# Kernel optimization log

Hardware: AMD Instinct MI355X
Metric: run time of the kernel (lower is better)

## Reference

```python
import jax, jax.numpy as jnp
import numpy as np

N = 16384
HID = 256
MI = 128
POS_PER_NODE = 4
TEMP = 0.5


def setup_inputs() -> dict:
    key = jax.random.key(0)
    k1, k2, k3, k4 = jax.random.split(key, 4)
    h_v1 = jax.random.normal(k1, (N, HID), dtype=jnp.float32)
    h_v2 = jax.random.normal(k2, (N, HID), dtype=jnp.float32)
    W = jax.random.normal(k3, (HID, MI), dtype=jnp.float32) * (1.0 / np.sqrt(HID))
    b = jnp.zeros((MI,), dtype=jnp.float32)
    # 4 positives per row -> every row has a nonzero positive count
    pos_row = jnp.repeat(jnp.arange(N, dtype=jnp.int32), POS_PER_NODE)
    pos_col = jax.random.randint(k4, (N * POS_PER_NODE,), 0, N, dtype=jnp.int32)
    return {"h_v1": h_v1, "h_v2": h_v2, "W": W, "b": b,
            "pos_row": pos_row, "pos_col": pos_col}


def _l2norm(x):
    return x / jnp.linalg.norm(x, axis=-1, keepdims=True)


def _cal_loss_mi(e1, e2, pos_row, pos_col):
    # sim_mat[i,j] = <e1_i, e2_j> / T   (N x N, the big intermediate)
    sim = jnp.einsum('ik,jk->ij', e1, e2) / TEMP
    sim = sim - jax.lax.stop_gradient(jnp.max(sim, axis=1, keepdims=True))
    sim = jnp.exp(sim)
    sim_pos = sim[pos_row, pos_col]                      # [E] gather
    row_sum = jnp.sum(sim, axis=1)                       # [N]
    pos_sum = jax.ops.segment_sum(sim_pos, pos_row, num_segments=N)
    denom = (row_sum - pos_sum)[pos_row]                 # [E]
    log_lv = jnp.log(sim_pos / denom)                    # [E]
    pos_cnt = jax.ops.segment_sum(jnp.ones_like(sim_pos), pos_row, num_segments=N)
    per_row = jax.ops.segment_sum(log_lv, pos_row, num_segments=N) / pos_cnt
    return -jnp.mean(per_row)


def reference(h_v1, h_v2, W, b, pos_row, pos_col):
    p1 = _l2norm(jax.nn.relu(h_v1 @ W + b))
    p2 = _l2norm(jax.nn.relu(h_v2 @ W + b))
    loss = 0.5 * (_cal_loss_mi(p1, p2, pos_row, pos_col)
                  + _cal_loss_mi(p2, p1, pos_row, pos_col))
    return loss
```

## Files before the change

### kernel.cpp

```cpp
#include <hip/hip_runtime.h>

typedef unsigned short ushort_t;
typedef unsigned int uint32;
typedef __attribute__((ext_vector_type(8))) short short8;
typedef __attribute__((ext_vector_type(4))) float f32x4;
typedef __attribute__((ext_vector_type(2))) float f32x2;

#define HID 256
#define MI 128
#define ALPHA 2.8853900817779268f
#define LN2F 0.69314718055994531f

__device__ __forceinline__ float bflo(uint32 u) { return __uint_as_float(u << 16); }
__device__ __forceinline__ float bfhi(uint32 u) { return __uint_as_float(u & 0xffff0000u); }
__device__ __forceinline__ ushort_t f2bf(float f) {
  uint32 u = __float_as_uint(f);
  u += 0x7fffu + ((u >> 16) & 1u);
  return (ushort_t)(u >> 16);
}

__global__ __launch_bounds__(256) void prep_kernel(
    const float* __restrict__ W, ushort_t* __restrict__ Wtb,
    float* __restrict__ fbase, int nz, float* __restrict__ out)
{
  int idx = blockIdx.x * 256 + threadIdx.x;
  if (idx < HID * MI) {
    int k = idx >> 7, nn = idx & 127;
    Wtb[nn * HID + k] = f2bf(W[k * MI + nn]);
  }
  if (idx < nz) fbase[idx] = 0.f;
  if (idx == 0) out[0] = 0.f;
}

__global__ __launch_bounds__(256) void proj_kernel(
    const float* __restrict__ h1, const float* __restrict__ h2,
    const ushort_t* __restrict__ Wtb, const float* __restrict__ b,
    ushort_t* __restrict__ p1b, ushort_t* __restrict__ p2b, int n)
{
  __shared__ __align__(16) unsigned char hb[64 * 512];
  int t = threadIdx.x;
  int lane = t & 63, w = t >> 6;
  int lr = lane & 15, lg = lane >> 4;
  long R0 = (long)blockIdx.x * 64;
  const float* src = (R0 < n) ? (h1 + R0 * HID) : (h2 + (R0 - n) * HID);
  ushort_t* dst = (R0 < n) ? (p1b + R0 * MI) : (p2b + (R0 - n) * MI);
  float scale = (R0 < n) ? ALPHA : 1.0f;

  float bb[8];
  #pragma unroll
  for (int ch = 0; ch < 8; ++ch) bb[ch] = b[ch * 16 + lr];

  const float4* g4 = (const float4*)src;
  #pragma unroll
  for (int i = 0; i < 16; ++i) {
    int idx4 = i * 256 + t;
    float4 v = g4[idx4];
    int row = idx4 >> 6;
    int k0 = (idx4 & 63) * 4;
    int gr = k0 >> 3;
    int off = row * 512 + ((gr ^ (row & 15)) << 4) + (k0 & 7) * 2;
    uint32 lo = (uint32)f2bf(v.x) | ((uint32)f2bf(v.y) << 16);
    uint32 hi = (uint32)f2bf(v.z) | ((uint32)f2bf(v.w) << 16);
    uint2 pk; pk.x = lo; pk.y = hi;
    *(uint2*)(hb + off) = pk;
  }
  __syncthreads();

  short8 afr[8];
  #pragma unroll
  for (int kt = 0; kt < 8; ++kt) {
    int row = w * 16 + lr;
    int g = kt * 4 + lg;
    afr[kt] = *(const short8*)(hb + row * 512 + ((g ^ (row & 15)) << 4));
  }

  f32x4 acc[8];
  #pragma unroll
  for (int ch = 0; ch < 8; ++ch) acc[ch] = (f32x4){0.f, 0.f, 0.f, 0.f};
  #pragma unroll
  for (int ch = 0; ch < 8; ++ch) {
    #pragma unroll
    for (int kt = 0; kt < 8; ++kt) {
      short8 bf = *(const short8*)(Wtb + (size_t)(ch * 16 + lr) * HID + kt * 32 + lg * 8);
      acc[ch] = __builtin_amdgcn_mfma_f32_16x16x32_bf16(afr[kt], bf, acc[ch], 0, 0, 0);
    }
  }

  #pragma unroll
  for (int r = 0; r < 4; ++r) {
    float v[8];
    float ss = 0.f;
    #pragma unroll
    for (int ch = 0; ch < 8; ++ch) {
      v[ch] = fmaxf(acc[ch][r] + bb[ch], 0.f);
      ss += v[ch] * v[ch];
    }
    ss += __shfl_xor(ss, 1, 64);
    ss += __shfl_xor(ss, 2, 64);
    ss += __shfl_xor(ss, 4, 64);
    ss += __shfl_xor(ss, 8, 64);
    float rn = rsqrtf(ss) * scale;
    int row = w * 16 + lg * 4 + r;
    #pragma unroll
    for (int ch = 0; ch < 8; ++ch)
      dst[(size_t)row * MI + ch * 16 + lr] = f2bf(v[ch] * rn);
  }
}

__global__ __launch_bounds__(512, 4) void sim_kernel(
    const ushort_t* __restrict__ p1b, const ushort_t* __restrict__ p2b,
    float* __restrict__ rowsum, float* __restrict__ colsum)
{
  __shared__ __align__(16) unsigned char ldsB[32768];
  __shared__ float colacc[1024];
  int t = threadIdx.x;
  int lane = t & 63, w = t >> 6;
  int lr = lane & 15, lg = lane >> 4;
  int rowbase = blockIdx.y * 256 + w * 32;
  int jbase = blockIdx.x * 1024;

  uint4 st0, st1;
  int g0 = t, g1 = t + 512;
  int row0 = g0 >> 4, gs0 = g0 & 15;
  int row1 = g1 >> 4, gs1 = g1 & 15;

  auto load_stage = [&](int jt) {
    int j0 = jbase + jt * 64;
    st0 = *(const uint4*)(p2b + (size_t)(j0 + row0) * MI + (gs0 << 3));
    st1 = *(const uint4*)(p2b + (size_t)(j0 + row1) * MI + (gs1 << 3));
  };
  auto write_stage = [&](int buf) {
    *(uint4*)(ldsB + buf * 16384 + row0 * 256 + ((gs0 ^ (row0 & 15)) << 4)) = st0;
    *(uint4*)(ldsB + buf * 16384 + row1 * 256 + ((gs1 ^ (row1 & 15)) << 4)) = st1;
  };

  load_stage(0);

  short8 afr[2][4];
  #pragma unroll
  for (int rt = 0; rt < 2; ++rt)
    #pragma unroll
    for (int kt = 0; kt < 4; ++kt)
      afr[rt][kt] = *(const short8*)(p1b + (size_t)(rowbase + rt * 16 + lr) * MI + kt * 32 + lg * 8);

  colacc[t] = 0.f;
  colacc[512 + t] = 0.f;

  f32x2 rs2[2][2];
  #pragma unroll
  for (int rt = 0; rt < 2; ++rt) {
    rs2[rt][0] = (f32x2){0.f, 0.f};
    rs2[rt][1] = (f32x2){0.f, 0.f};
  }

  write_stage(0);
  __syncthreads();

  for (int jt = 0; jt < 16; ++jt) {
    int cur = jt & 1;
    if (jt + 1 < 16) load_stage(jt + 1);
    const unsigned char* B = ldsB + cur * 16384;

    #pragma unroll
    for (int ch = 0; ch < 4; ++ch) {
      f32x4 acc[2];
      acc[0] = (f32x4){0.f, 0.f, 0.f, 0.f};
      acc[1] = (f32x4){0.f, 0.f, 0.f, 0.f};
      #pragma unroll
      for (int kt = 0; kt < 4; ++kt) {
        int ncol = ch * 16 + lr;
        int g = kt * 4 + lg;
        short8 bf = *(const short8*)(B + ncol * 256 + ((g ^ (ncol & 15)) << 4));
        acc[0] = __builtin_amdgcn_mfma_f32_16x16x32_bf16(afr[0][kt], bf, acc[0], 0, 0, 0);
        acc[1] = __builtin_amdgcn_mfma_f32_16x16x32_bf16(afr[1][kt], bf, acc[1], 0, 0, 0);
      }
      f32x2 cs2 = (f32x2){0.f, 0.f};
      #pragma unroll
      for (int rt = 0; rt < 2; ++rt) {
        f32x2 e01, e23;
        e01[0] = __builtin_amdgcn_exp2f(acc[rt][0]);
        e01[1] = __builtin_amdgcn_exp2f(acc[rt][1]);
        e23[0] = __builtin_amdgcn_exp2f(acc[rt][2]);
        e23[1] = __builtin_amdgcn_exp2f(acc[rt][3]);
        rs2[rt][0] += e01;
        rs2[rt][1] += e23;
        cs2 += e01;
        cs2 += e23;
      }
      float csum = cs2[0] + cs2[1];
      csum += __shfl_xor(csum, 16, 64);
      csum += __shfl_xor(csum, 32, 64);
      if (lg == 0) atomicAdd(&colacc[jt * 64 + ch * 16 + lr], csum);
    }
    if (jt + 1 < 16) write_stage(1 - cur);
    __syncthreads();
  }

  #pragma unroll
  for (int rt = 0; rt < 2; ++rt)
    #pragma unroll
    for (int j = 0; j < 2; ++j)
      #pragma unroll
      for (int s = 0; s < 2; ++s) {
        float v = rs2[rt][j][s];
        v += __shfl_xor(v, 1, 64);
        v += __shfl_xor(v, 2, 64);
        v += __shfl_xor(v, 4, 64);
        v += __shfl_xor(v, 8, 64);
        if (lr == 0) atomicAdd(&rowsum[rowbase + rt * 16 + lg * 4 + j * 2 + s], v);
      }

  atomicAdd(&colsum[jbase + t], colacc[t]);
  atomicAdd(&colsum[jbase + 512 + t], colacc[512 + t]);
}

__global__ __launch_bounds__(256) void edge_kernel(
    const int* __restrict__ pos_row, const int* __restrict__ pos_col,
    const ushort_t* __restrict__ p1b, const ushort_t* __restrict__ p2b,
    float* __restrict__ psum1, float* __restrict__ psum2,
    float* __restrict__ srow1, float* __restrict__ srow2,
    float* __restrict__ cntb, int E)
{
  int tid = blockIdx.x * 256 + threadIdx.x;
  int e = tid >> 2, q = tid & 3;
  if (e >= E) return;
  int r = pos_row[e], c = pos_col[e];
  const uint4* a1 = (const uint4*)(p1b + (size_t)r * MI) + q * 4;
  const uint4* b1 = (const uint4*)(p2b + (size_t)c * MI) + q * 4;
  const uint4* a2 = (const uint4*)(p1b + (size_t)c * MI) + q * 4;
  const uint4* b2 = (const uint4*)(p2b + (size_t)r * MI) + q * 4;
  float d1 = 0.f, d2 = 0.f;
  #pragma unroll
  for (int it = 0; it < 4; ++it) {
    uint4 x = a1[it], y = b1[it];
    d1 += bflo(x.x) * bflo(y.x) + bfhi(x.x) * bfhi(y.x);
    d1 += bflo(x.y) * bflo(y.y) + bfhi(x.y) * bfhi(y.y);
    d1 += bflo(x.z) * bflo(y.z) + bfhi(x.z) * bfhi(y.z);
    d1 += bflo(x.w) * bflo(y.w) + bfhi(x.w) * bfhi(y.w);
    uint4 u = a2[it], v = b2[it];
    d2 += bflo(u.x) * bflo(v.x) + bfhi(u.x) * bfhi(v.x);
    d2 += bflo(u.y) * bflo(v.y) + bfhi(u.y) * bfhi(v.y);
    d2 += bflo(u.z) * bflo(v.z) + bfhi(u.z) * bfhi(v.z);
    d2 += bflo(u.w) * bflo(v.w) + bfhi(u.w) * bfhi(v.w);
  }
  d1 += __shfl_xor(d1, 1, 64);
  d1 += __shfl_xor(d1, 2, 64);
  d2 += __shfl_xor(d2, 1, 64);
  d2 += __shfl_xor(d2, 2, 64);
  if (q == 0) {
    float e1 = __builtin_amdgcn_exp2f(d1);
    float e2 = __builtin_amdgcn_exp2f(d2);
    atomicAdd(&psum1[r], e1);
    atomicAdd(&srow1[r], d1 * LN2F);
    atomicAdd(&psum2[r], e2);
    atomicAdd(&srow2[r], d2 * LN2F);
    atomicAdd(&cntb[r], 1.0f);
  }
}

__global__ __launch_bounds__(256) void finalize_kernel(
    const float* __restrict__ rowsum, const float* __restrict__ colsum,
    const float* __restrict__ psum1, const float* __restrict__ psum2,
    const float* __restrict__ srow1, const float* __restrict__ srow2,
    const float* __restrict__ cntb, float* __restrict__ out, int n)
{
  __shared__ float sred[4];
  int r = blockIdx.x * 256 + threadIdx.x;
  float local = 0.f;
  if (r < n) {
    float inv = 1.0f / cntb[r];
    float d1 = rowsum[r] - psum1[r];
    float d2 = colsum[r] - psum2[r];
    local = srow1[r] * inv - __builtin_amdgcn_logf(d1) * LN2F
          + srow2[r] * inv - __builtin_amdgcn_logf(d2) * LN2F;
  }
  #pragma unroll
  for (int m = 1; m <= 32; m <<= 1) local += __shfl_xor(local, m, 64);
  int lane = threadIdx.x & 63, wv = threadIdx.x >> 6;
  if (lane == 0) sred[wv] = local;
  __syncthreads();
  if (threadIdx.x == 0) {
    float tot = sred[0] + sred[1] + sred[2] + sred[3];
    atomicAdd(out, -tot / (2.0f * n));
  }
}

extern "C" void kernel_launch(void* const* d_in, const int* in_sizes, int n_in,
                              void* d_out, int out_size, void* d_ws, size_t ws_size,
                              hipStream_t stream)
{
  const float* h1 = (const float*)d_in[0];
  const float* h2 = (const float*)d_in[1];
  const float* W  = (const float*)d_in[2];
  const float* b  = (const float*)d_in[3];
  const int* pos_row = (const int*)d_in[4];
  const int* pos_col = (const int*)d_in[5];
  int n = in_sizes[0] / HID;
  int E = in_sizes[4];
  float* out = (float*)d_out;

  char* ws = (char*)d_ws;
  ushort_t* p1b = (ushort_t*)ws;
  ushort_t* p2b = p1b + (size_t)n * MI;
  float* fbase  = (float*)(ws + (size_t)2 * n * MI * sizeof(ushort_t));
  float* rowsum = fbase;
  float* colsum = rowsum + n;
  float* psum1  = colsum + n;
  float* psum2  = psum1 + n;
  float* srow1  = psum2 + n;
  float* srow2  = srow1 + n;
  float* cntb   = srow2 + n;
  ushort_t* Wtb = (ushort_t*)(cntb + n);

  int nz = 7 * n;
  prep_kernel<<<(nz + 255) / 256, 256, 0, stream>>>(W, Wtb, fbase, nz, out);
  proj_kernel<<<2 * n / 64, 256, 0, stream>>>(h1, h2, Wtb, b, p1b, p2b, n);
  dim3 g2(n / 1024, n / 256);
  sim_kernel<<<g2, 512, 0, stream>>>(p1b, p2b, rowsum, colsum);
  edge_kernel<<<(E * 4 + 255) / 256, 256, 0, stream>>>(pos_row, pos_col, p1b, p2b,
                                                       psum1, psum2, srow1, srow2, cntb, E);
  finalize_kernel<<<(n + 255) / 256, 256, 0, stream>>>(rowsum, colsum, psum1, psum2,
                                                       srow1, srow2, cntb, out, n);
}
```

Before: 206.7 us.

## Fuse edge pass into sim kernel and double rows per wave

Removes the separate edge kernel and runs the positive-pair dot products in an extra row of blocks inside the similarity kernel, so they overlap with the main tile work. The accumulator zeroing moves from the prep kernel into the projection kernel, which shrinks the prep launch. Each wave in the similarity kernel now computes 64 rows instead of 32, reusing each staged B fragment across four MFMA row tiles. In exchange, register pressure rises and the similarity grid has half as many blocks, which could reduce occupancy and latency hiding.

```diff
diff --git a/kernel.cpp b/kernel.cpp
--- a/kernel.cpp
+++ b/kernel.cpp
@@ -21,24 +21,27 @@
 
 __global__ __launch_bounds__(256) void prep_kernel(
     const float* __restrict__ W, ushort_t* __restrict__ Wtb,
-    float* __restrict__ fbase, int nz, float* __restrict__ out)
+    float* __restrict__ out)
 {
   int idx = blockIdx.x * 256 + threadIdx.x;
   if (idx < HID * MI) {
     int k = idx >> 7, nn = idx & 127;
     Wtb[nn * HID + k] = f2bf(W[k * MI + nn]);
   }
-  if (idx < nz) fbase[idx] = 0.f;
   if (idx == 0) out[0] = 0.f;
 }
 
 __global__ __launch_bounds__(256) void proj_kernel(
     const float* __restrict__ h1, const float* __restrict__ h2,
     const ushort_t* __restrict__ Wtb, const float* __restrict__ b,
-    ushort_t* __restrict__ p1b, ushort_t* __restrict__ p2b, int n)
+    ushort_t* __restrict__ p1b, ushort_t* __restrict__ p2b, int n,
+    float* __restrict__ fbase, int nz)
 {
   __shared__ __align__(16) unsigned char hb[64 * 512];
   int t = threadIdx.x;
+  int gid = blockIdx.x * 256 + t;
+  if (gid < nz) fbase[gid] = 0.f;
+
   int lane = t & 63, w = t >> 6;
   int lr = lane & 15, lg = lane >> 4;
   long R0 = (long)blockIdx.x * 64;
@@ -107,21 +110,66 @@
   }
 }
 
-__global__ __launch_bounds__(512, 4) void sim_kernel(
+__global__ __launch_bounds__(512, 4) void sim_edge_kernel(
     const ushort_t* __restrict__ p1b, const ushort_t* __restrict__ p2b,
-    float* __restrict__ rowsum, float* __restrict__ colsum)
+    float* __restrict__ rowsum, float* __restrict__ colsum,
+    const int* __restrict__ pos_row, const int* __restrict__ pos_col,
+    float* __restrict__ psum1, float* __restrict__ psum2,
+    float* __restrict__ srow1, float* __restrict__ srow2,
+    float* __restrict__ cntb, int E)
 {
   __shared__ __align__(16) unsigned char ldsB[32768];
   __shared__ float colacc[1024];
   int t = threadIdx.x;
+
+  if (blockIdx.y == gridDim.y - 1) {
+    int lim = E * 4;
+    for (int idx = blockIdx.x * 512 + t; idx < lim; idx += 16 * 512) {
+      int e = idx >> 2, q = idx & 3;
+      int r = pos_row[e], c = pos_col[e];
+      const uint4* a1 = (const uint4*)(p1b + (size_t)r * MI) + q * 4;
+      const uint4* b1 = (const uint4*)(p2b + (size_t)c * MI) + q * 4;
+      const uint4* a2 = (const uint4*)(p1b + (size_t)c * MI) + q * 4;
+      const uint4* b2 = (const uint4*)(p2b + (size_t)r * MI) + q * 4;
+      float d1 = 0.f, d2 = 0.f;
+      #pragma unroll
+      for (int it = 0; it < 4; ++it) {
+        uint4 x = a1[it], y = b1[it];
+        d1 += bflo(x.x) * bflo(y.x) + bfhi(x.x) * bfhi(y.x);
+        d1 += bflo(x.y) * bflo(y.y) + bfhi(x.y) * bfhi(y.y);
+        d1 += bflo(x.z) * bflo(y.z) + bfhi(x.z) * bfhi(y.z);
+        d1 += bflo(x.w) * bflo(y.w) + bfhi(x.w) * bfhi(y.w);
+        uint4 u = a2[it], v = b2[it];
+        d2 += bflo(u.x) * bflo(v.x) + bfhi(u.x) * bfhi(v.x);
+        d2 += bflo(u.y) * bflo(v.y) + bfhi(u.y) * bfhi(v.y);
+        d2 += bflo(u.z) * bflo(v.z) + bfhi(u.z) * bfhi(v.z);
+        d2 += bflo(u.w) * bflo(v.w) + bfhi(u.w) * bfhi(v.w);
+      }
+      d1 += __shfl_xor(d1, 1, 64);
+      d1 += __shfl_xor(d1, 2, 64);
+      d2 += __shfl_xor(d2, 1, 64);
+      d2 += __shfl_xor(d2, 2, 64);
+      if (q == 0) {
+        float e1 = __builtin_amdgcn_exp2f(d1);
+        float e2 = __builtin_amdgcn_exp2f(d2);
+        atomicAdd(&psum1[r], e1);
+        atomicAdd(&srow1[r], d1 * LN2F);
+        atomicAdd(&psum2[r], e2);
+        atomicAdd(&srow2[r], d2 * LN2F);
+        atomicAdd(&cntb[r], 1.0f);
+      }
+    }
+    return;
+  }
+
   int lane = t & 63, w = t >> 6;
   int lr = lane & 15, lg = lane >> 4;
-  int rowbase = blockIdx.y * 256 + w * 32;
+  int rowbase = blockIdx.y * 512 + w * 64;
   int jbase = blockIdx.x * 1024;
 
   uint4 st0, st1;
-  int g0 = t, g1 = t + 512;
-  int row0 = g0 >> 4, gs0 = g0 & 15;
+  int row0 = t >> 4, gs0 = t & 15;
+  int g1 = t + 512;
   int row1 = g1 >> 4, gs1 = g1 & 15;
 
   auto load_stage = [&](int jt) {
@@ -136,9 +184,9 @@
 
   load_stage(0);
 
-  short8 afr[2][4];
-  #pragma unroll
-  for (int rt = 0; rt < 2; ++rt)
+  short8 afr[4][4];
+  #pragma unroll
+  for (int rt = 0; rt < 4; ++rt)
     #pragma unroll
     for (int kt = 0; kt < 4; ++kt)
       afr[rt][kt] = *(const short8*)(p1b + (size_t)(rowbase + rt * 16 + lr) * MI + kt * 32 + lg * 8);
@@ -146,9 +194,9 @@
   colacc[t] = 0.f;
   colacc[512 + t] = 0.f;
 
-  f32x2 rs2[2][2];
-  #pragma unroll
-  for (int rt = 0; rt < 2; ++rt) {
+  f32x2 rs2[4][2];
+  #pragma unroll
+  for (int rt = 0; rt < 4; ++rt) {
     rs2[rt][0] = (f32x2){0.f, 0.f};
     rs2[rt][1] = (f32x2){0.f, 0.f};
   }
@@ -163,20 +211,21 @@
 
     #pragma unroll
     for (int ch = 0; ch < 4; ++ch) {
-      f32x4 acc[2];
-      acc[0] = (f32x4){0.f, 0.f, 0.f, 0.f};
-      acc[1] = (f32x4){0.f, 0.f, 0.f, 0.f};
+      f32x4 acc[4];
+      #pragma unroll
+      for (int rt = 0; rt < 4; ++rt) acc[rt] = (f32x4){0.f, 0.f, 0.f, 0.f};
       #pragma unroll
       for (int kt = 0; kt < 4; ++kt) {
         int ncol = ch * 16 + lr;
         int g = kt * 4 + lg;
         short8 bf = *(const short8*)(B + ncol * 256 + ((g ^ (ncol & 15)) << 4));
-        acc[0] = __builtin_amdgcn_mfma_f32_16x16x32_bf16(afr[0][kt], bf, acc[0], 0, 0, 0);
-        acc[1] = __builtin_amdgcn_mfma_f32_16x16x32_bf16(afr[1][kt], bf, acc[1], 0, 0, 0);
+        #pragma unroll
+        for (int rt = 0; rt < 4; ++rt)
+          acc[rt] = __builtin_amdgcn_mfma_f32_16x16x32_bf16(afr[rt][kt], bf, acc[rt], 0, 0, 0);
       }
       f32x2 cs2 = (f32x2){0.f, 0.f};
       #pragma unroll
-      for (int rt = 0; rt < 2; ++rt) {
+      for (int rt = 0; rt < 4; ++rt) {
         f32x2 e01, e23;
         e01[0] = __builtin_amdgcn_exp2f(acc[rt][0]);
         e01[1] = __builtin_amdgcn_exp2f(acc[rt][1]);
@@ -197,7 +246,7 @@
   }
 
   #pragma unroll
-  for (int rt = 0; rt < 2; ++rt)
+  for (int rt = 0; rt < 4; ++rt)
     #pragma unroll
     for (int j = 0; j < 2; ++j)
       #pragma unroll
@@ -212,50 +261,6 @@
 
   atomicAdd(&colsum[jbase + t], colacc[t]);
   atomicAdd(&colsum[jbase + 512 + t], colacc[512 + t]);
-}
-
-__global__ __launch_bounds__(256) void edge_kernel(
-    const int* __restrict__ pos_row, const int* __restrict__ pos_col,
-    const ushort_t* __restrict__ p1b, const ushort_t* __restrict__ p2b,
-    float* __restrict__ psum1, float* __restrict__ psum2,
-    float* __restrict__ srow1, float* __restrict__ srow2,
-    float* __restrict__ cntb, int E)
-{
-  int tid = blockIdx.x * 256 + threadIdx.x;
-  int e = tid >> 2, q = tid & 3;
-  if (e >= E) return;
-  int r = pos_row[e], c = pos_col[e];
-  const uint4* a1 = (const uint4*)(p1b + (size_t)r * MI) + q * 4;
-  const uint4* b1 = (const uint4*)(p2b + (size_t)c * MI) + q * 4;
-  const uint4* a2 = (const uint4*)(p1b + (size_t)c * MI) + q * 4;
-  const uint4* b2 = (const uint4*)(p2b + (size_t)r * MI) + q * 4;
-  float d1 = 0.f, d2 = 0.f;
-  #pragma unroll
-  for (int it = 0; it < 4; ++it) {
-    uint4 x = a1[it], y = b1[it];
-    d1 += bflo(x.x) * bflo(y.x) + bfhi(x.x) * bfhi(y.x);
-    d1 += bflo(x.y) * bflo(y.y) + bfhi(x.y) * bfhi(y.y);
-    d1 += bflo(x.z) * bflo(y.z) + bfhi(x.z) * bfhi(y.z);
-    d1 += bflo(x.w) * bflo(y.w) + bfhi(x.w) * bfhi(y.w);
-    uint4 u = a2[it], v = b2[it];
-    d2 += bflo(u.x) * bflo(v.x) + bfhi(u.x) * bfhi(v.x);
-    d2 += bflo(u.y) * bflo(v.y) + bfhi(u.y) * bfhi(v.y);
-    d2 += bflo(u.z) * bflo(v.z) + bfhi(u.z) * bfhi(v.z);
-    d2 += bflo(u.w) * bflo(v.w) + bfhi(u.w) * bfhi(v.w);
-  }
-  d1 += __shfl_xor(d1, 1, 64);
-  d1 += __shfl_xor(d1, 2, 64);
-  d2 += __shfl_xor(d2, 1, 64);
-  d2 += __shfl_xor(d2, 2, 64);
-  if (q == 0) {
-    float e1 = __builtin_amdgcn_exp2f(d1);
-    float e2 = __builtin_amdgcn_exp2f(d2);
-    atomicAdd(&psum1[r], e1);
-    atomicAdd(&srow1[r], d1 * LN2F);
-    atomicAdd(&psum2[r], e2);
-    atomicAdd(&srow2[r], d2 * LN2F);
-    atomicAdd(&cntb[r], 1.0f);
-  }
 }
 
 __global__ __launch_bounds__(256) void finalize_kernel(
@@ -313,12 +318,13 @@
   ushort_t* Wtb = (ushort_t*)(cntb + n);
 
   int nz = 7 * n;
-  prep_kernel<<<(nz + 255) / 256, 256, 0, stream>>>(W, Wtb, fbase, nz, out);
-  proj_kernel<<<2 * n / 64, 256, 0, stream>>>(h1, h2, Wtb, b, p1b, p2b, n);
-  dim3 g2(n / 1024, n / 256);
-  sim_kernel<<<g2, 512, 0, stream>>>(p1b, p2b, rowsum, colsum);
-  edge_kernel<<<(E * 4 + 255) / 256, 256, 0, stream>>>(pos_row, pos_col, p1b, p2b,
-                                                       psum1, psum2, srow1, srow2, cntb, E);
+  prep_kernel<<<(HID * MI + 255) / 256, 256, 0, stream>>>(W, Wtb, out);
+  proj_kernel<<<2 * n / 64, 256, 0, stream>>>(h1, h2, Wtb, b, p1b, p2b, n,
+                                              fbase, nz);
+  dim3 g2(n / 1024, n / 512 + 1);
+  sim_edge_kernel<<<g2, 512, 0, stream>>>(p1b, p2b, rowsum, colsum,
+                                          pos_row, pos_col,
+                                          psum1, psum2, srow1, srow2, cntb, E);
   finalize_kernel<<<(n + 255) / 256, 256, 0, stream>>>(rowsum, colsum, psum1, psum2,
                                                        srow1, srow2, cntb, out, n);
 }
```

Result: slower. 478.7 us (+131.6%).
